# Optimization experiments

Measured on AMD Instinct MI355X. Metric: run time of the kernel, lower is better.

Reference implementation:

```python
import jax, jax.numpy as jnp
import numpy as np

B, H, S, D = 4, 16, 2048, 64
TEMPERATURE = 8.0  # sqrt(D)
MASK_FILL = -1e9


def setup_inputs() -> dict:
    key = jax.random.key(0)
    kq, kk, kv, km = jax.random.split(key, 4)
    q = jax.random.normal(kq, (B, H, S, D), dtype=jnp.float32)
    k = jax.random.normal(kk, (B, H, S, D), dtype=jnp.float32)
    v = jax.random.normal(kv, (B, H, S, D), dtype=jnp.float32)
    mask = jax.random.randint(km, (B, 1, 1, S), 0, 2, dtype=jnp.int32)
    return {"q": q, "k": k, "v": v, "mask": mask}


def reference(q, k, v, mask):
    # attn = (q / temperature) @ k^T  -> [B,H,S,S]
    attn = jnp.einsum('bhqd,bhkd->bhqk', q / TEMPERATURE, k)
    # mask-fill where mask == 0 (broadcasts over heads/query dim)
    attn = jnp.where(mask == 0, MASK_FILL, attn)
    # dropout is identity at inference (training=None in the original)
    # NOTE: the original module applies NO softmax; faithful reproduction.
    output = jnp.einsum('bhqk,bhkd->bhqd', attn, v)
    return (output, attn)
```

## Files before the change

### kernel.cpp

```cpp
#include <hip/hip_runtime.h>

constexpr int Bn = 4, Hn = 16, Sn = 2048, Dn = 64;
constexpr float MASK_FILL = -1e9f;

typedef __bf16 bf16x8 __attribute__((ext_vector_type(8)));
typedef __bf16 bf16x4 __attribute__((ext_vector_type(4)));
typedef float  f32x4  __attribute__((ext_vector_type(4)));
typedef int    i32x4  __attribute__((ext_vector_type(4)));

#define KSTRIDE 72
#define VSTRIDE 136

#define BARRIER_LGKM() asm volatile("s_waitcnt lgkmcnt(0)\n\ts_barrier" ::: "memory")

__global__ __launch_bounds__(256, 2) void attn_fused(
    const float* __restrict__ qg, const float* __restrict__ kg,
    const float* __restrict__ vg, const int* __restrict__ maskg,
    float* __restrict__ outg, float* __restrict__ attng)
{
  __shared__ __align__(16) __bf16 lds_k [128 * KSTRIDE];
  __shared__ __align__(16) __bf16 lds_vt[ 64 * VSTRIDE];
  __shared__ __align__(16) __bf16 lds_qs[128 * KSTRIDE];
  __shared__ __align__(16) int    lds_m [Sn];

  const int fid  = blockIdx.y * gridDim.x + blockIdx.x;
  const int nf   = ((fid & 7) << 7) | (fid >> 3);
  const int qt   = nf & 15;
  const int bh   = nf >> 4;
  const int b    = bh >> 4;
  const int tid  = threadIdx.x;
  const int wave = tid >> 6;
  const int lane = tid & 63;
  const int quad = lane >> 4;
  const int l16  = lane & 15;

  const size_t hbase = (size_t)bh * Sn * Dn;
  const float* qp = qg + hbase + (size_t)qt * 128 * Dn;
  float* attnp = attng + (size_t)bh * Sn * Sn + (size_t)qt * 128 * (size_t)Sn;

  const int r0 = tid >> 4;
  const int c  = (tid & 15) << 2;

  {
    const int* mp = maskg + b * Sn;
    *(i32x4*)&lds_m[tid * 8]     = *(const i32x4*)(mp + tid * 8);
    *(i32x4*)&lds_m[tid * 8 + 4] = *(const i32x4*)(mp + tid * 8 + 4);
  }

#pragma unroll
  for (int i = 0; i < 8; ++i) {
    const int r = r0 + (i << 4);
    f32x4 val = __builtin_nontemporal_load((const f32x4*)(qp + r * Dn + c));
    bf16x4 pk;
    pk.x = (__bf16)(val.x * 0.125f);
    pk.y = (__bf16)(val.y * 0.125f);
    pk.z = (__bf16)(val.z * 0.125f);
    pk.w = (__bf16)(val.w * 0.125f);
    *(bf16x4*)&lds_qs[r * KSTRIDE + c] = pk;
  }

  f32x4 kpre[8], vpre[8];
  const float* kbase = kg + hbase;
  const float* vbase = vg + hbase;
#pragma unroll
  for (int i = 0; i < 8; ++i) {
    const int r = r0 + (i << 4);
    kpre[i] = *(const f32x4*)(kbase + r * Dn + c);
    vpre[i] = *(const f32x4*)(vbase + r * Dn + c);
  }

  BARRIER_LGKM();

  bf16x8 qa[2][2];
#pragma unroll
  for (int qs = 0; qs < 2; ++qs)
#pragma unroll
    for (int ks = 0; ks < 2; ++ks)
      qa[qs][ks] = *(const bf16x8*)&lds_qs[(wave * 32 + qs * 16 + l16) * KSTRIDE + ks * 32 + quad * 8];

  __bf16* sbuf = &lds_qs[wave * 32 * KSTRIDE];

  f32x4 oacc[2][4];
#pragma unroll
  for (int qs = 0; qs < 2; ++qs)
#pragma unroll
    for (int ds = 0; ds < 4; ++ds)
      oacc[qs][ds] = (f32x4){0.f, 0.f, 0.f, 0.f};

  for (int kt = 0; kt < 16; ++kt) {
    BARRIER_LGKM();

#pragma unroll
    for (int i = 0; i < 8; ++i) {
      const int r = r0 + (i << 4);
      f32x4 kv = kpre[i];
      bf16x4 pk;
      pk.x = (__bf16)kv.x; pk.y = (__bf16)kv.y;
      pk.z = (__bf16)kv.z; pk.w = (__bf16)kv.w;
      *(bf16x4*)&lds_k[r * KSTRIDE + c] = pk;
      f32x4 vv = vpre[i];
      lds_vt[(c + 0) * VSTRIDE + r] = (__bf16)vv.x;
      lds_vt[(c + 1) * VSTRIDE + r] = (__bf16)vv.y;
      lds_vt[(c + 2) * VSTRIDE + r] = (__bf16)vv.z;
      lds_vt[(c + 3) * VSTRIDE + r] = (__bf16)vv.w;
    }

    BARRIER_LGKM();

    if (kt < 15) {
      const float* kp = kbase + (size_t)((kt + 1) * 128) * Dn;
      const float* vp = vbase + (size_t)((kt + 1) * 128) * Dn;
#pragma unroll
      for (int i = 0; i < 8; ++i) {
        const int r = r0 + (i << 4);
        kpre[i] = *(const f32x4*)(kp + r * Dn + c);
        vpre[i] = *(const f32x4*)(vp + r * Dn + c);
      }
    }

    f32x4 sacc[2][8];
#pragma unroll
    for (int ns = 0; ns < 8; ++ns) {
      bf16x8 ka0 = *(const bf16x8*)&lds_k[(ns * 16 + l16) * KSTRIDE +      quad * 8];
      bf16x8 ka1 = *(const bf16x8*)&lds_k[(ns * 16 + l16) * KSTRIDE + 32 + quad * 8];
#pragma unroll
      for (int qs = 0; qs < 2; ++qs) {
        f32x4 acc = (f32x4){0.f, 0.f, 0.f, 0.f};
        acc = __builtin_amdgcn_mfma_f32_16x16x32_bf16(ka0, qa[qs][0], acc, 0, 0, 0);
        acc = __builtin_amdgcn_mfma_f32_16x16x32_bf16(ka1, qa[qs][1], acc, 0, 0, 0);
        sacc[qs][ns] = acc;
      }
    }

#pragma unroll
    for (int ns = 0; ns < 8; ++ns) {
      const i32x4 m4 = *(const i32x4*)&lds_m[kt * 128 + ns * 16 + quad * 4];
#pragma unroll
      for (int qs = 0; qs < 2; ++qs) {
        f32x4 sv = sacc[qs][ns];
        sv.x = m4.x ? sv.x : MASK_FILL;
        sv.y = m4.y ? sv.y : MASK_FILL;
        sv.z = m4.z ? sv.z : MASK_FILL;
        sv.w = m4.w ? sv.w : MASK_FILL;
        sacc[qs][ns] = sv;
        const int row = wave * 32 + qs * 16 + l16;
        __builtin_nontemporal_store(sv,
            (f32x4*)(attnp + (size_t)row * Sn + kt * 128 + ns * 16 + quad * 4));
      }
    }

#pragma unroll
    for (int half = 0; half < 2; ++half) {
#pragma unroll
      for (int ns4 = 0; ns4 < 4; ++ns4) {
        const int ns = half * 4 + ns4;
#pragma unroll
        for (int qs = 0; qs < 2; ++qs) {
          f32x4 sv = sacc[qs][ns];
          bf16x4 sb;
          sb.x = (__bf16)sv.x; sb.y = (__bf16)sv.y;
          sb.z = (__bf16)sv.z; sb.w = (__bf16)sv.w;
          *(bf16x4*)&sbuf[(qs * 16 + l16) * KSTRIDE + ns4 * 16 + quad * 4] = sb;
        }
      }
      asm volatile("" ::: "memory");
#pragma unroll
      for (int ks = 0; ks < 2; ++ks) {
        bf16x8 sb0 = *(const bf16x8*)&sbuf[(     l16) * KSTRIDE + ks * 32 + quad * 8];
        bf16x8 sb1 = *(const bf16x8*)&sbuf[(16 + l16) * KSTRIDE + ks * 32 + quad * 8];
#pragma unroll
        for (int ds = 0; ds < 4; ++ds) {
          bf16x8 va = *(const bf16x8*)&lds_vt[(ds * 16 + l16) * VSTRIDE + half * 64 + ks * 32 + quad * 8];
          oacc[0][ds] = __builtin_amdgcn_mfma_f32_16x16x32_bf16(va, sb0, oacc[0][ds], 0, 0, 0);
          oacc[1][ds] = __builtin_amdgcn_mfma_f32_16x16x32_bf16(va, sb1, oacc[1][ds], 0, 0, 0);
        }
      }
      asm volatile("" ::: "memory");
    }
  }

  float* op = outg + hbase + (size_t)qt * 128 * Dn;
#pragma unroll
  for (int qs = 0; qs < 2; ++qs)
#pragma unroll
    for (int ds = 0; ds < 4; ++ds) {
      const int row = wave * 32 + qs * 16 + l16;
      __builtin_nontemporal_store(oacc[qs][ds],
          (f32x4*)(op + (size_t)row * Dn + ds * 16 + quad * 4));
    }
}

extern "C" void kernel_launch(void* const* d_in, const int* in_sizes, int n_in,
                              void* d_out, int out_size, void* d_ws, size_t ws_size,
                              hipStream_t stream) {
  const float* q    = (const float*)d_in[0];
  const float* k    = (const float*)d_in[1];
  const float* v    = (const float*)d_in[2];
  const int*   mask = (const int*)d_in[3];
  float* out  = (float*)d_out;
  float* attn = out + (size_t)Bn * Hn * Sn * Dn;

  dim3 grid(Sn / 128, Bn * Hn);
  attn_fused<<<grid, 256, 0, stream>>>(q, k, v, mask, out, attn);
}
```

Baseline: 1.302 ms.

## Vectorize V transpose into LDS and interleave masking/stores with QK MFMAs

Changes the V prefetch mapping so each thread loads 8 consecutive rows, which lets the transposed V tile be written to LDS as 16-byte bf16x8 stores instead of scalar 2-byte stores. Fuses the mask application and the attn global store into the QK^T MFMA loop so stores issue as scores are produced. Also switches attn stores from nontemporal to normal stores. These target LDS write overhead and try to overlap the large attn output write with compute. The normal stores may pollute cache, and the new V load pattern is less coalesced per instruction.

```diff
diff --git a/kernel.cpp b/kernel.cpp
--- a/kernel.cpp
+++ b/kernel.cpp
@@ -64,9 +64,8 @@
   const float* vbase = vg + hbase;
 #pragma unroll
   for (int i = 0; i < 8; ++i) {
-    const int r = r0 + (i << 4);
-    kpre[i] = *(const f32x4*)(kbase + r * Dn + c);
-    vpre[i] = *(const f32x4*)(vbase + r * Dn + c);
+    kpre[i] = *(const f32x4*)(kbase + (r0 + (i << 4)) * Dn + c);
+    vpre[i] = *(const f32x4*)(vbase + (r0 * 8 + i) * Dn + c);
   }
 
   BARRIER_LGKM();
@@ -98,11 +97,14 @@
       pk.x = (__bf16)kv.x; pk.y = (__bf16)kv.y;
       pk.z = (__bf16)kv.z; pk.w = (__bf16)kv.w;
       *(bf16x4*)&lds_k[r * KSTRIDE + c] = pk;
-      f32x4 vv = vpre[i];
-      lds_vt[(c + 0) * VSTRIDE + r] = (__bf16)vv.x;
-      lds_vt[(c + 1) * VSTRIDE + r] = (__bf16)vv.y;
-      lds_vt[(c + 2) * VSTRIDE + r] = (__bf16)vv.z;
-      lds_vt[(c + 3) * VSTRIDE + r] = (__bf16)vv.w;
+    }
+#pragma unroll
+    for (int j = 0; j < 4; ++j) {
+      bf16x8 t;
+#pragma unroll
+      for (int i = 0; i < 8; ++i)
+        t[i] = (__bf16)vpre[i][j];
+      *(bf16x8*)&lds_vt[(c + j) * VSTRIDE + r0 * 8] = t;
     }
 
     BARRIER_LGKM();
@@ -112,9 +114,8 @@
       const float* vp = vbase + (size_t)((kt + 1) * 128) * Dn;
 #pragma unroll
       for (int i = 0; i < 8; ++i) {
-        const int r = r0 + (i << 4);
-        kpre[i] = *(const f32x4*)(kp + r * Dn + c);
-        vpre[i] = *(const f32x4*)(vp + r * Dn + c);
+        kpre[i] = *(const f32x4*)(kp + (r0 + (i << 4)) * Dn + c);
+        vpre[i] = *(const f32x4*)(vp + (r0 * 8 + i) * Dn + c);
       }
     }
 
@@ -123,29 +124,19 @@
     for (int ns = 0; ns < 8; ++ns) {
       bf16x8 ka0 = *(const bf16x8*)&lds_k[(ns * 16 + l16) * KSTRIDE +      quad * 8];
       bf16x8 ka1 = *(const bf16x8*)&lds_k[(ns * 16 + l16) * KSTRIDE + 32 + quad * 8];
+      const i32x4 m4 = *(const i32x4*)&lds_m[kt * 128 + ns * 16 + quad * 4];
 #pragma unroll
       for (int qs = 0; qs < 2; ++qs) {
         f32x4 acc = (f32x4){0.f, 0.f, 0.f, 0.f};
         acc = __builtin_amdgcn_mfma_f32_16x16x32_bf16(ka0, qa[qs][0], acc, 0, 0, 0);
         acc = __builtin_amdgcn_mfma_f32_16x16x32_bf16(ka1, qa[qs][1], acc, 0, 0, 0);
+        acc.x = m4.x ? acc.x : MASK_FILL;
+        acc.y = m4.y ? acc.y : MASK_FILL;
+        acc.z = m4.z ? acc.z : MASK_FILL;
+        acc.w = m4.w ? acc.w : MASK_FILL;
         sacc[qs][ns] = acc;
-      }
-    }
-
-#pragma unroll
-    for (int ns = 0; ns < 8; ++ns) {
-      const i32x4 m4 = *(const i32x4*)&lds_m[kt * 128 + ns * 16 + quad * 4];
-#pragma unroll
-      for (int qs = 0; qs < 2; ++qs) {
-        f32x4 sv = sacc[qs][ns];
-        sv.x = m4.x ? sv.x : MASK_FILL;
-        sv.y = m4.y ? sv.y : MASK_FILL;
-        sv.z = m4.z ? sv.z : MASK_FILL;
-        sv.w = m4.w ? sv.w : MASK_FILL;
-        sacc[qs][ns] = sv;
         const int row = wave * 32 + qs * 16 + l16;
-        __builtin_nontemporal_store(sv,
-            (f32x4*)(attnp + (size_t)row * Sn + kt * 128 + ns * 16 + quad * 4));
+        *(f32x4*)(attnp + (size_t)row * Sn + kt * 128 + ns * 16 + quad * 4) = acc;
       }
     }
 
```

Measured after the change: 1.298 ms. No clear change (-0.3%).
